# Optimization experiments

Measured on AMD Instinct MI355X. Metric: run time of the kernel, lower is better.

Reference implementation:

```python
import jax, jax.numpy as jnp
from jax import lax
import numpy as np

EPS = 1e-5

def _layer_norm(x):
    mu = jnp.mean(x, axis=-1, keepdims=True)
    var = jnp.mean(jnp.square(x - mu), axis=-1, keepdims=True)
    return (x - mu) / jnp.sqrt(var + EPS)

def setup_inputs() -> dict:
    key = jax.random.key(0)
    k1, k2 = jax.random.split(key)
    B, S, D = 2, 2048, 128
    n_hashes, num_buckets = 8, 32
    x = jax.random.normal(k1, (B, S, D), dtype=jnp.float32)
    input_mask = jnp.ones((B, S), dtype=jnp.float32)
    # random rotations for LSH hashing: (B, D, n_hashes, num_buckets//2)
    rotations = jax.random.normal(k2, (B, D, n_hashes, num_buckets // 2), dtype=jnp.float32)
    return {"x": x, "input_mask": input_mask, "rotations": rotations, "num_buckets": num_buckets}

def reference(x, input_mask, rotations, num_buckets):
    B, S, D = x.shape
    xn = _layer_norm(x)
    # LSH hashing: rotate, concat +/-, argmax over bucket axis -> (B, n_hashes, S)
    rot = jnp.einsum('bnd,bdhk->bhnk', xn, rotations)
    rot = jnp.concatenate([rot, -rot], axis=-1)
    buckets = jnp.argmax(rot, axis=-1)
    xm = xn * input_mask[..., None]
    # source loop reassigns round_buckets each hash round; only the last survives
    round_buckets = buckets[:, -1, :]  # (B, S)
    scale = 1.0 / jnp.sqrt(jnp.asarray(D, dtype=x.dtype))
    def body(out, bucket_id):
        m = (round_buckets == bucket_id).astype(xm.dtype)[..., None]  # (B,S,1)
        cb = xm * m  # zero out tokens outside the bucket (faithful to source)
        scores = jnp.einsum('bsd,btd->bst', cb, cb) * scale  # (B,S,S)
        attn = jax.nn.softmax(scores, axis=-1)
        out = out + jnp.einsum('bst,btd->bsd', attn, cb) * m
        return out, None
    out, _ = lax.scan(body, jnp.zeros_like(xm), jnp.arange(num_buckets))
    return out
```

## Files before the change

### kernel.cpp

```cpp
#include <hip/hip_runtime.h>
#include <math.h>

constexpr int B = 2;
constexpr int S = 2048;
constexpr int D = 128;
constexpr int NH = 8;
constexpr int NK = 16;
constexpr int NB = 32;
constexpr float EPS = 1e-5f;
constexpr float SCALE = 0.08838834764831845f;

constexpr int MAXN = 192;
constexpr int KP   = 136;
constexpr int TP   = 200;
constexpr int QSPLIT = 4;

typedef __attribute__((ext_vector_type(8))) short bf16x8;
typedef __attribute__((ext_vector_type(4))) float f32x4;

__device__ __forceinline__ ushort f2bf(float f) {
    uint u = __float_as_uint(f);
    u += 0x7FFFu + ((u >> 16) & 1u);
    return (ushort)(u >> 16);
}

__global__ __launch_bounds__(256) void ln_hash_kernel(
    const float* __restrict__ x, const float* __restrict__ mask,
    const float* __restrict__ rot, ushort* __restrict__ xmb,
    int* __restrict__ bucket, float* __restrict__ selfp)
{
    const int wave = threadIdx.x >> 6;
    const int lane = threadIdx.x & 63;
    const int row  = blockIdx.x * 4 + wave;
    const int b    = row >> 11;

    const float v0 = x[(size_t)row * D + lane];
    const float v1 = x[(size_t)row * D + lane + 64];

    float s = v0 + v1;
    #pragma unroll
    for (int off = 32; off > 0; off >>= 1) s += __shfl_xor(s, off, 64);
    const float mu = s * (1.0f / 128.0f);

    const float c0 = v0 - mu, c1 = v1 - mu;
    float s2 = c0 * c0 + c1 * c1;
    #pragma unroll
    for (int off = 32; off > 0; off >>= 1) s2 += __shfl_xor(s2, off, 64);
    const float rstd = 1.0f / sqrtf(s2 * (1.0f / 128.0f) + EPS);

    const float xn0 = c0 * rstd, xn1 = c1 * rstd;
    const float mk = mask[row];
    xmb[(size_t)row * D + lane]      = f2bf(xn0 * mk);
    xmb[(size_t)row * D + lane + 64] = f2bf(xn1 * mk);

    const float* r0 = rot + (((size_t)(b * D + lane)) * NH + (NH - 1)) * NK;
    const float* r1 = rot + (((size_t)(b * D + lane + 64)) * NH + (NH - 1)) * NK;
    float racc[NK];
    #pragma unroll
    for (int k = 0; k < NK; ++k) racc[k] = xn0 * r0[k] + xn1 * r1[k];
    #pragma unroll
    for (int k = 0; k < NK; ++k) {
        float t = racc[k];
        #pragma unroll
        for (int off = 32; off > 0; off >>= 1) t += __shfl_xor(t, off, 64);
        racc[k] = t;
    }

    float best = racc[0]; int bi = 0;
    #pragma unroll
    for (int k = 1; k < NK; ++k) if (racc[k] > best) { best = racc[k]; bi = k; }
    #pragma unroll
    for (int k = 0; k < NK; ++k) if (-racc[k] > best) { best = -racc[k]; bi = k + NK; }

    if (lane == 0) {
        bucket[row] = bi;
        selfp[row] = SCALE * s2 * rstd * rstd * mk * mk;
    }
}

__global__ __launch_bounds__(256) void attn_kernel(
    const ushort* __restrict__ xmb, const int* __restrict__ bucket,
    const float* __restrict__ selfp, float* __restrict__ out)
{
    const int bg   = blockIdx.x >> 2;
    const int qs   = blockIdx.x & 3;
    const int b    = bg >> 5;
    const int beta = bg & 31;
    const int tid  = threadIdx.x;
    const int lane = tid & 63;
    const int wave = tid >> 6;
    const int col  = lane & 15;
    const int quad = lane >> 4;

    __shared__ __align__(16) ushort Kb[MAXN * KP];
    __shared__ __align__(16) ushort KTb[D * TP];
    __shared__ __align__(16) float  w[16 * TP];
    __shared__ __align__(16) ushort Pt[16 * TP];
    __shared__ int   idx[MAXN];
    __shared__ float scratch[256];
    __shared__ float Mrow[16], invrow[16];
    __shared__ int   wsum[4];

    const int base = b * S;
    const int4* bp = (const int4*)(bucket + base);
    const int4 v0 = bp[tid * 2];
    const int4 v1 = bp[tid * 2 + 1];
    int m0 = (v0.x == beta) | ((v0.y == beta) << 1) | ((v0.z == beta) << 2) |
             ((v0.w == beta) << 3) | ((v1.x == beta) << 4) | ((v1.y == beta) << 5) |
             ((v1.z == beta) << 6) | ((v1.w == beta) << 7);
    const int cntl = __popc(m0);

    int inc = cntl;
    #pragma unroll
    for (int off = 1; off < 64; off <<= 1) {
        const int t = __shfl_up(inc, off, 64);
        if (lane >= off) inc += t;
    }
    if (lane == 63) wsum[wave] = inc;
    __syncthreads();
    int start = inc - cntl;
    #pragma unroll
    for (int wv = 0; wv < 4; ++wv) if (wv < wave) start += wsum[wv];
    const int ntot = wsum[0] + wsum[1] + wsum[2] + wsum[3];
    const int n = min(ntot, MAXN);

    {
        const int t0 = tid * 8;
        int p = start;
        #pragma unroll
        for (int k = 0; k < 8; ++k)
            if ((m0 >> k) & 1) { if (p < MAXN) idx[p] = t0 + k; ++p; }
    }
    __syncthreads();
    if (n == 0) return;
    const int npad32 = (n + 31) & ~31;

    for (int c = tid; c < n * 16; c += 256) {
        const int i = c >> 4, ch = c & 15;
        *(bf16x8*)&Kb[i * KP + ch * 8] =
            *(const bf16x8*)(xmb + (size_t)(base + idx[i]) * D + ch * 8);
    }
    __syncthreads();

    for (int e = tid; e < n * D; e += 256) {
        const int j = e >> 7, d = e & 127;
        KTb[d * TP + j] = Kb[j * KP + d];
    }
    for (int e = tid; e < D * 32; e += 256) {
        const int d = e >> 5, j = n + (e & 31);
        if (j < npad32) KTb[d * TP + j] = 0;
    }
    for (int e = tid; e < 16 * 32; e += 256) {
        const int r = e >> 5, j = n + (e & 31);
        if (j < npad32) Pt[r * TP + j] = 0;
    }
    __syncthreads();

    for (int qt = qs; qt * 16 < n; qt += QSPLIT) {
        const int q0 = qt * 16;
        const int rows = min(16, n - q0);

        for (int kt = wave; kt * 16 < n; kt += 4) {
            const int J0 = kt * 16;
            f32x4 acc = {0.f, 0.f, 0.f, 0.f};
            #pragma unroll
            for (int ks = 0; ks < 4; ++ks) {
                const bf16x8 a = *(const bf16x8*)&Kb[(q0 + col) * KP + quad * 8 + ks * 32];
                const bf16x8 bb = *(const bf16x8*)&Kb[(J0 + col) * KP + quad * 8 + ks * 32];
                acc = __builtin_amdgcn_mfma_f32_16x16x32_bf16(a, bb, acc, 0, 0, 0);
            }
            #pragma unroll
            for (int r = 0; r < 4; ++r)
                w[(quad * 4 + r) * TP + J0 + col] = acc[r] * SCALE;
        }
        __syncthreads();

        if (tid < rows)
            w[tid * TP + q0 + tid] = selfp[base + idx[q0 + tid]];
        __syncthreads();

        {
            const int r = tid >> 4, g = tid & 15;
            float pm = 0.0f;
            if (r < rows)
                for (int j = g; j < n; j += 16) pm = fmaxf(pm, w[r * TP + j]);
            scratch[tid] = pm;
            __syncthreads();
            if (tid < 16 && tid < rows) {
                float m = scratch[tid * 16];
                #pragma unroll
                for (int k = 1; k < 16; ++k) m = fmaxf(m, scratch[tid * 16 + k]);
                Mrow[tid] = m;
            }
            __syncthreads();
            float ps = 0.0f;
            if (r < rows) {
                const float M = Mrow[r];
                for (int j = g; j < n; j += 16) {
                    const float e = expf(w[r * TP + j] - M);
                    Pt[r * TP + j] = f2bf(e);
                    ps += e;
                }
            }
            scratch[tid] = ps;
            __syncthreads();
            if (tid < 16 && tid < rows) {
                float ssum = 0.0f;
                #pragma unroll
                for (int k = 0; k < 16; ++k) ssum += scratch[tid * 16 + k];
                ssum += (float)(S - n) * expf(-Mrow[tid]);
                invrow[tid] = 1.0f / ssum;
            }
            __syncthreads();
        }

        for (int dt = wave; dt < 8; dt += 4) {
            f32x4 acc = {0.f, 0.f, 0.f, 0.f};
            for (int ks = 0; ks < npad32 / 32; ++ks) {
                const bf16x8 a = *(const bf16x8*)&Pt[col * TP + ks * 32 + quad * 8];
                const bf16x8 bb = *(const bf16x8*)&KTb[(dt * 16 + col) * TP + ks * 32 + quad * 8];
                acc = __builtin_amdgcn_mfma_f32_16x16x32_bf16(a, bb, acc, 0, 0, 0);
            }
            #pragma unroll
            for (int r = 0; r < 4; ++r) {
                const int rr = quad * 4 + r;
                if (rr < rows)
                    out[(size_t)(base + idx[q0 + rr]) * D + dt * 16 + col] =
                        acc[r] * invrow[rr];
            }
        }
        __syncthreads();
    }
}

extern "C" void kernel_launch(void* const* d_in, const int* in_sizes, int n_in,
                              void* d_out, int out_size, void* d_ws, size_t ws_size,
                              hipStream_t stream) {
    const float* x    = (const float*)d_in[0];
    const float* mask = (const float*)d_in[1];
    const float* rot  = (const float*)d_in[2];

    char* ws = (char*)d_ws;
    ushort* xmb  = (ushort*)ws;                  ws += (size_t)B * S * D * sizeof(ushort);
    int*    bkt  = (int*)ws;                     ws += (size_t)B * S * sizeof(int);
    float*  self = (float*)ws;
    float*  out  = (float*)d_out;

    ln_hash_kernel<<<B * S / 4, 256, 0, stream>>>(x, mask, rot, xmb, bkt, self);
    attn_kernel<<<B * NB * QSPLIT, 256, 0, stream>>>(xmb, bkt, self, out);
}
```

Baseline: 79.23 us.

## Drop K transpose buffer, double query split, use shuffle-based softmax reductions

The attention kernel no longer builds a transposed copy of K in shared memory. The PV matmul gathers B-operand elements with strided reads from the row-major K buffer, which cuts LDS use and allows two blocks per CU. The query split grows from 4 to 8 blocks per bucket, and blocks with no query tile exit early. The softmax max/sum reductions use 16-lane shuffles instead of shared scratch and several barriers, and the self-score diagonal is written inside the QK loop. LayerNorm fuses the mean and sum-of-squares reductions (E[x²]−mu² form, slightly less stable) and loads rotations as float4. Strided scalar LDS gathers may add bank conflicts and issue cost.

```diff
diff --git a/kernel.cpp b/kernel.cpp
--- a/kernel.cpp
+++ b/kernel.cpp
@@ -13,7 +13,7 @@
 constexpr int MAXN = 192;
 constexpr int KP   = 136;
 constexpr int TP   = 200;
-constexpr int QSPLIT = 4;
+constexpr int QSPLIT = 8;
 
 typedef __attribute__((ext_vector_type(8))) short bf16x8;
 typedef __attribute__((ext_vector_type(4))) float f32x4;
@@ -37,27 +37,34 @@
     const float v0 = x[(size_t)row * D + lane];
     const float v1 = x[(size_t)row * D + lane + 64];
 
-    float s = v0 + v1;
-    #pragma unroll
-    for (int off = 32; off > 0; off >>= 1) s += __shfl_xor(s, off, 64);
-    const float mu = s * (1.0f / 128.0f);
-
-    const float c0 = v0 - mu, c1 = v1 - mu;
-    float s2 = c0 * c0 + c1 * c1;
-    #pragma unroll
-    for (int off = 32; off > 0; off >>= 1) s2 += __shfl_xor(s2, off, 64);
-    const float rstd = 1.0f / sqrtf(s2 * (1.0f / 128.0f) + EPS);
-
-    const float xn0 = c0 * rstd, xn1 = c1 * rstd;
+    float s  = v0 + v1;
+    float s2 = v0 * v0 + v1 * v1;
+    #pragma unroll
+    for (int off = 32; off > 0; off >>= 1) {
+        s  += __shfl_xor(s,  off, 64);
+        s2 += __shfl_xor(s2, off, 64);
+    }
+    const float mu      = s * (1.0f / 128.0f);
+    const float central = s2 - 128.0f * mu * mu;
+    const float rstd    = 1.0f / sqrtf(central * (1.0f / 128.0f) + EPS);
+
+    const float xn0 = (v0 - mu) * rstd, xn1 = (v1 - mu) * rstd;
     const float mk = mask[row];
     xmb[(size_t)row * D + lane]      = f2bf(xn0 * mk);
     xmb[(size_t)row * D + lane + 64] = f2bf(xn1 * mk);
 
-    const float* r0 = rot + (((size_t)(b * D + lane)) * NH + (NH - 1)) * NK;
-    const float* r1 = rot + (((size_t)(b * D + lane + 64)) * NH + (NH - 1)) * NK;
+    const float4* r0 = (const float4*)(rot + (((size_t)(b * D + lane)) * NH + (NH - 1)) * NK);
+    const float4* r1 = (const float4*)(rot + (((size_t)(b * D + lane + 64)) * NH + (NH - 1)) * NK);
     float racc[NK];
     #pragma unroll
-    for (int k = 0; k < NK; ++k) racc[k] = xn0 * r0[k] + xn1 * r1[k];
+    for (int q = 0; q < 4; ++q) {
+        const float4 a = r0[q];
+        const float4 c = r1[q];
+        racc[q * 4 + 0] = xn0 * a.x + xn1 * c.x;
+        racc[q * 4 + 1] = xn0 * a.y + xn1 * c.y;
+        racc[q * 4 + 2] = xn0 * a.z + xn1 * c.z;
+        racc[q * 4 + 3] = xn0 * a.w + xn1 * c.w;
+    }
     #pragma unroll
     for (int k = 0; k < NK; ++k) {
         float t = racc[k];
@@ -74,16 +81,16 @@
 
     if (lane == 0) {
         bucket[row] = bi;
-        selfp[row] = SCALE * s2 * rstd * rstd * mk * mk;
-    }
-}
-
-__global__ __launch_bounds__(256) void attn_kernel(
+        selfp[row] = SCALE * central * rstd * rstd * mk * mk;
+    }
+}
+
+__global__ __launch_bounds__(256, 2) void attn_kernel(
     const ushort* __restrict__ xmb, const int* __restrict__ bucket,
     const float* __restrict__ selfp, float* __restrict__ out)
 {
-    const int bg   = blockIdx.x >> 2;
-    const int qs   = blockIdx.x & 3;
+    const int bg   = blockIdx.x >> 3;
+    const int qs   = blockIdx.x & 7;
     const int b    = bg >> 5;
     const int beta = bg & 31;
     const int tid  = threadIdx.x;
@@ -93,21 +100,19 @@
     const int quad = lane >> 4;
 
     __shared__ __align__(16) ushort Kb[MAXN * KP];
-    __shared__ __align__(16) ushort KTb[D * TP];
     __shared__ __align__(16) float  w[16 * TP];
     __shared__ __align__(16) ushort Pt[16 * TP];
     __shared__ int   idx[MAXN];
-    __shared__ float scratch[256];
-    __shared__ float Mrow[16], invrow[16];
+    __shared__ float invrow[16];
     __shared__ int   wsum[4];
 
     const int base = b * S;
     const int4* bp = (const int4*)(bucket + base);
-    const int4 v0 = bp[tid * 2];
-    const int4 v1 = bp[tid * 2 + 1];
-    int m0 = (v0.x == beta) | ((v0.y == beta) << 1) | ((v0.z == beta) << 2) |
-             ((v0.w == beta) << 3) | ((v1.x == beta) << 4) | ((v1.y == beta) << 5) |
-             ((v1.z == beta) << 6) | ((v1.w == beta) << 7);
+    const int4 u0 = bp[tid * 2];
+    const int4 u1 = bp[tid * 2 + 1];
+    int m0 = (u0.x == beta) | ((u0.y == beta) << 1) | ((u0.z == beta) << 2) |
+             ((u0.w == beta) << 3) | ((u1.x == beta) << 4) | ((u1.y == beta) << 5) |
+             ((u1.z == beta) << 6) | ((u1.w == beta) << 7);
     const int cntl = __popc(m0);
 
     int inc = cntl;
@@ -123,6 +128,8 @@
     for (int wv = 0; wv < 4; ++wv) if (wv < wave) start += wsum[wv];
     const int ntot = wsum[0] + wsum[1] + wsum[2] + wsum[3];
     const int n = min(ntot, MAXN);
+
+    if (qs * 16 >= n) return;
 
     {
         const int t0 = tid * 8;
@@ -132,7 +139,6 @@
             if ((m0 >> k) & 1) { if (p < MAXN) idx[p] = t0 + k; ++p; }
     }
     __syncthreads();
-    if (n == 0) return;
     const int npad32 = (n + 31) & ~31;
 
     for (int c = tid; c < n * 16; c += 256) {
@@ -140,15 +146,12 @@
         *(bf16x8*)&Kb[i * KP + ch * 8] =
             *(const bf16x8*)(xmb + (size_t)(base + idx[i]) * D + ch * 8);
     }
-    __syncthreads();
-
-    for (int e = tid; e < n * D; e += 256) {
-        const int j = e >> 7, d = e & 127;
-        KTb[d * TP + j] = Kb[j * KP + d];
-    }
-    for (int e = tid; e < D * 32; e += 256) {
-        const int d = e >> 5, j = n + (e & 31);
-        if (j < npad32) KTb[d * TP + j] = 0;
+    {
+        const bf16x8 z = {0, 0, 0, 0, 0, 0, 0, 0};
+        for (int e = tid; e < 32 * 16; e += 256) {
+            const int j = n + (e >> 4), ch = e & 15;
+            if (j < npad32) *(bf16x8*)&Kb[j * KP + ch * 8] = z;
+        }
     }
     for (int e = tid; e < 16 * 32; e += 256) {
         const int r = e >> 5, j = n + (e & 31);
@@ -165,60 +168,53 @@
             f32x4 acc = {0.f, 0.f, 0.f, 0.f};
             #pragma unroll
             for (int ks = 0; ks < 4; ++ks) {
-                const bf16x8 a = *(const bf16x8*)&Kb[(q0 + col) * KP + quad * 8 + ks * 32];
+                const bf16x8 a  = *(const bf16x8*)&Kb[(q0 + col) * KP + quad * 8 + ks * 32];
                 const bf16x8 bb = *(const bf16x8*)&Kb[(J0 + col) * KP + quad * 8 + ks * 32];
                 acc = __builtin_amdgcn_mfma_f32_16x16x32_bf16(a, bb, acc, 0, 0, 0);
             }
-            #pragma unroll
-            for (int r = 0; r < 4; ++r)
-                w[(quad * 4 + r) * TP + J0 + col] = acc[r] * SCALE;
+            float selfv = 0.0f;
+            if (J0 == q0 && q0 + col < n) selfv = selfp[base + idx[q0 + col]];
+            #pragma unroll
+            for (int r = 0; r < 4; ++r) {
+                const int i = quad * 4 + r;
+                float v = acc[r] * SCALE;
+                if (J0 == q0 && col == i) v = selfv;
+                w[i * TP + J0 + col] = v;
+            }
         }
         __syncthreads();
 
-        if (tid < rows)
-            w[tid * TP + q0 + tid] = selfp[base + idx[q0 + tid]];
-        __syncthreads();
-
         {
-            const int r = tid >> 4, g = tid & 15;
+            const int r = wave * 4 + quad;
+            const int g = col;
             float pm = 0.0f;
             if (r < rows)
                 for (int j = g; j < n; j += 16) pm = fmaxf(pm, w[r * TP + j]);
-            scratch[tid] = pm;
-            __syncthreads();
-            if (tid < 16 && tid < rows) {
-                float m = scratch[tid * 16];
-                #pragma unroll
-                for (int k = 1; k < 16; ++k) m = fmaxf(m, scratch[tid * 16 + k]);
-                Mrow[tid] = m;
-            }
-            __syncthreads();
+            #pragma unroll
+            for (int off = 8; off > 0; off >>= 1) pm = fmaxf(pm, __shfl_xor(pm, off, 16));
             float ps = 0.0f;
             if (r < rows) {
-                const float M = Mrow[r];
                 for (int j = g; j < n; j += 16) {
-                    const float e = expf(w[r * TP + j] - M);
+                    const float e = __expf(w[r * TP + j] - pm);
                     Pt[r * TP + j] = f2bf(e);
                     ps += e;
                 }
             }
-            scratch[tid] = ps;
-            __syncthreads();
-            if (tid < 16 && tid < rows) {
-                float ssum = 0.0f;
-                #pragma unroll
-                for (int k = 0; k < 16; ++k) ssum += scratch[tid * 16 + k];
-                ssum += (float)(S - n) * expf(-Mrow[tid]);
-                invrow[tid] = 1.0f / ssum;
-            }
-            __syncthreads();
-        }
+            #pragma unroll
+            for (int off = 8; off > 0; off >>= 1) ps += __shfl_xor(ps, off, 16);
+            if (r < rows && g == 0)
+                invrow[r] = 1.0f / (ps + (float)(S - n) * __expf(-pm));
+        }
+        __syncthreads();
 
         for (int dt = wave; dt < 8; dt += 4) {
             f32x4 acc = {0.f, 0.f, 0.f, 0.f};
             for (int ks = 0; ks < npad32 / 32; ++ks) {
                 const bf16x8 a = *(const bf16x8*)&Pt[col * TP + ks * 32 + quad * 8];
-                const bf16x8 bb = *(const bf16x8*)&KTb[(dt * 16 + col) * TP + ks * 32 + quad * 8];
+                bf16x8 bb;
+                #pragma unroll
+                for (int e = 0; e < 8; ++e)
+                    bb[e] = (short)Kb[(ks * 32 + quad * 8 + e) * KP + dt * 16 + col];
                 acc = __builtin_amdgcn_mfma_f32_16x16x32_bf16(a, bb, acc, 0, 0, 0);
             }
             #pragma unroll
```

After: 75.94 us (median of 2 runs). -4.1%, faster.
